# Performance work log

Measured on AMD Instinct MI355X. Metric: run time of the kernel, lower is better.

Reference implementation:

```python
import jax, jax.numpy as jnp
import numpy as np

E = 1024      # embed_size
H = 16        # num_heads
DH = E // H   # head_size = 64
B = 4
T = 2048


def _layernorm(x, g, b, eps=1e-5):
    mu = jnp.mean(x, axis=-1, keepdims=True)
    var = jnp.var(x, axis=-1, keepdims=True)
    return (x - mu) * jax.lax.rsqrt(var + eps) * g + b


def setup_inputs() -> dict:
    key = jax.random.key(0)
    ks = jax.random.split(key, 12)
    s = 0.02
    return {
        "x": jax.random.normal(ks[0], (B, T, E), dtype=jnp.float32),
        "ln1_g": jnp.ones((E,), jnp.float32),
        "ln1_b": jnp.zeros((E,), jnp.float32),
        "Wq": jax.random.normal(ks[1], (H, E, DH), jnp.float32) * s,
        "Wk": jax.random.normal(ks[2], (H, E, DH), jnp.float32) * s,
        "Wv": jax.random.normal(ks[3], (H, E, DH), jnp.float32) * s,
        "Wp": jax.random.normal(ks[4], (E, E), jnp.float32) * s,
        "bp": jnp.zeros((E,), jnp.float32),
        "ln2_g": jnp.ones((E,), jnp.float32),
        "ln2_b": jnp.zeros((E,), jnp.float32),
        "W1": jax.random.normal(ks[5], (E, 4 * E), jnp.float32) * s,
        "b1": jnp.zeros((4 * E,), jnp.float32),
        "W2": jax.random.normal(ks[6], (4 * E, E), jnp.float32) * s,
        "b2": jnp.zeros((E,), jnp.float32),
    }


def reference(x, ln1_g, ln1_b, Wq, Wk, Wv, Wp, bp, ln2_g, ln2_b, W1, b1, W2, b2):
    # --- self-attention branch (pre-LN) ---
    h = _layernorm(x, ln1_g, ln1_b)
    q = jnp.einsum("bte,hed->bhtd", h, Wq)
    k = jnp.einsum("bte,hed->bhtd", h, Wk)
    v = jnp.einsum("bte,hed->bhtd", h, Wv)
    # NOTE: original scales by embed_size**-0.5 (C of the input), not head_size
    scale = jnp.float32(E) ** -0.5
    w = jnp.einsum("bhtd,bhsd->bhts", q, k) * scale  # [B,H,T,T]
    causal = jnp.tril(jnp.ones((T, T), dtype=bool))
    w = jnp.where(causal, w, -jnp.inf)
    w = jax.nn.softmax(w, axis=-1)
    att = jnp.einsum("bhts,bhsd->bhtd", w, v)        # [B,H,T,DH]
    att = jnp.transpose(att, (0, 2, 1, 3)).reshape(B, T, E)  # concat heads
    x = x + att @ Wp + bp
    # --- FFN branch (pre-LN) ---
    h2 = _layernorm(x, ln2_g, ln2_b)
    ff = jax.nn.relu(h2 @ W1 + b1) @ W2 + b2
    return x + ff
```

## Files before the change

kernel.cpp:

```cpp
#include <hip/hip_runtime.h>
#include <stdint.h>

#define DEV __device__ __forceinline__

typedef unsigned short u16;
typedef short s16x8 __attribute__((ext_vector_type(8)));
typedef u16 u16x4 __attribute__((ext_vector_type(4)));
typedef float f32x4 __attribute__((ext_vector_type(4)));

constexpr int Bc = 4, Tc = 2048, Ec = 1024, Hc = 16, DHc = 64, FFc = 4096;

DEV u16 f2bf(float f) {
    union { float f; uint32_t u; } v; v.f = f;
    uint32_t r = v.u + 0x7fffu + ((v.u >> 16) & 1u);
    return (u16)(r >> 16);
}
DEV float bf2f(u16 u) {
    union { uint32_t u; float f; } v; v.u = ((uint32_t)u) << 16;
    return v.f;
}

DEV void gload16(const void* g, void* l) {
    __builtin_amdgcn_global_load_lds((const __attribute__((address_space(1))) void*)g,
                                     (__attribute__((address_space(3))) void*)l, 16, 0, 0);
}

template <typename TIN>
__global__ __launch_bounds__(256) void transpose_conv(const TIN* __restrict__ in,
                                                      u16* __restrict__ out, int R, int C) {
    __shared__ float tile[32][33];
    int bz = blockIdx.z;
    in  += (size_t)bz * R * C;
    out += (size_t)bz * R * C;
    int c0 = blockIdx.x * 32, r0 = blockIdx.y * 32;
    int tx = threadIdx.x, ty = threadIdx.y;
#pragma unroll
    for (int i = 0; i < 4; i++) {
        int r = ty + 8 * i;
        float v;
        if constexpr (sizeof(TIN) == 4) v = ((const float*)in)[(size_t)(r0 + r) * C + c0 + tx];
        else                            v = bf2f(((const u16*)in)[(size_t)(r0 + r) * C + c0 + tx]);
        tile[r][tx] = v;
    }
    __syncthreads();
#pragma unroll
    for (int i = 0; i < 4; i++) {
        int c = ty + 8 * i;
        out[(size_t)(c0 + c) * R + r0 + tx] = f2bf(tile[tx][c]);
    }
}

__global__ __launch_bounds__(256) void ln_kernel(const float* __restrict__ x, const float* __restrict__ g,
                                                 const float* __restrict__ b, u16* __restrict__ out) {
    int row = blockIdx.x;
    const float4* xr = (const float4*)(x + (size_t)row * Ec);
    int t = threadIdx.x;
    float4 v = xr[t];
    float s = v.x + v.y + v.z + v.w;
    float ss = v.x * v.x + v.y * v.y + v.z * v.z + v.w * v.w;
#pragma unroll
    for (int off = 32; off > 0; off >>= 1) { s += __shfl_xor(s, off); ss += __shfl_xor(ss, off); }
    __shared__ float red[8];
    int wid = t >> 6;
    if ((t & 63) == 0) { red[wid] = s; red[4 + wid] = ss; }
    __syncthreads();
    s = red[0] + red[1] + red[2] + red[3];
    ss = red[4] + red[5] + red[6] + red[7];
    float mu = s * (1.f / Ec);
    float rs = rsqrtf(ss * (1.f / Ec) - mu * mu + 1e-5f);
    float4 gv = ((const float4*)g)[t], bv = ((const float4*)b)[t];
    u16x4 o;
    o[0] = f2bf((v.x - mu) * rs * gv.x + bv.x);
    o[1] = f2bf((v.y - mu) * rs * gv.y + bv.y);
    o[2] = f2bf((v.z - mu) * rs * gv.z + bv.z);
    o[3] = f2bf((v.w - mu) * rs * gv.w + bv.w);
    *(u16x4*)(out + (size_t)row * Ec + t * 4) = o;
}

template <int MODE>
__global__ __launch_bounds__(256) void gemm_kernel(const u16* __restrict__ A, const u16* __restrict__ Bt,
                                                   int K, int N,
                                                   u16* __restrict__ o0, u16* __restrict__ o1, u16* __restrict__ o2,
                                                   float* __restrict__ of, const float* __restrict__ bias,
                                                   const float* __restrict__ res) {
    __shared__ u16 As[128 * 32];
    __shared__ u16 Bs[128 * 32];
    int tm = blockIdx.y * 128, tn = blockIdx.x * 128;
    int tid = threadIdx.x;
    int w = tid >> 6, l = tid & 63;
    int wm = w >> 1, wn = w & 1;
    int q16 = l & 15, g = l >> 4;

    f32x4 acc[4][4];
#pragma unroll
    for (int i = 0; i < 4; i++)
#pragma unroll
        for (int j = 0; j < 4; j++) acc[i][j] = {0.f, 0.f, 0.f, 0.f};

    const u16* Aw0 = A + (size_t)(tm + w * 32 + (l >> 2)) * K + (l & 3) * 8;
    const u16* Aw1 = Aw0 + (size_t)16 * K;
    const u16* Bw0 = Bt + (size_t)(tn + w * 32 + (l >> 2)) * K + (l & 3) * 8;
    const u16* Bw1 = Bw0 + (size_t)16 * K;
    u16* Asw = As + (w * 32) * 32;
    u16* Bsw = Bs + (w * 32) * 32;

    for (int k0 = 0; k0 < K; k0 += 32) {
        gload16(Aw0 + k0, Asw);
        gload16(Aw1 + k0, Asw + 16 * 32);
        gload16(Bw0 + k0, Bsw);
        gload16(Bw1 + k0, Bsw + 16 * 32);
        asm volatile("s_waitcnt vmcnt(0)" ::: "memory");
        __syncthreads();
        s16x8 af[4], bf[4];
#pragma unroll
        for (int i = 0; i < 4; i++) {
            af[i] = *(const s16x8*)(As + (wm * 64 + i * 16 + q16) * 32 + g * 8);
            bf[i] = *(const s16x8*)(Bs + (wn * 64 + i * 16 + q16) * 32 + g * 8);
        }
#pragma unroll
        for (int i = 0; i < 4; i++)
#pragma unroll
            for (int j = 0; j < 4; j++)
                acc[i][j] = __builtin_amdgcn_mfma_f32_16x16x32_bf16(af[i], bf[j], acc[i][j], 0, 0, 0);
        __syncthreads();
    }

#pragma unroll
    for (int i = 0; i < 4; i++) {
        int m0 = tm + wm * 64 + i * 16 + g * 4;
#pragma unroll
        for (int j = 0; j < 4; j++) {
            int n = tn + wn * 64 + j * 16 + q16;
            if constexpr (MODE == 0) {
                int tensor = n >> 10, hh = (n >> 6) & 15, d = n & 63;
                u16* dst = tensor == 0 ? o0 : (tensor == 1 ? o1 : o2);
#pragma unroll
                for (int r = 0; r < 4; r++) {
                    int m = m0 + r;
                    int bb = m >> 11, tt = m & 2047;
                    dst[(((size_t)(bb * Hc + hh) * Tc + tt) << 6) + d] = f2bf(acc[i][j][r]);
                }
            } else if constexpr (MODE == 1) {
                float bv = bias[n];
#pragma unroll
                for (int r = 0; r < 4; r++) {
                    int m = m0 + r;
                    o0[(size_t)m * N + n] = f2bf(fmaxf(acc[i][j][r] + bv, 0.f));
                }
            } else {
                float bv = bias[n];
#pragma unroll
                for (int r = 0; r < 4; r++) {
                    int m = m0 + r;
                    of[(size_t)m * N + n] = acc[i][j][r] + bv + res[(size_t)m * N + n];
                }
            }
        }
    }
}

__global__ __launch_bounds__(256) void attn_kernel(const u16* __restrict__ q, const u16* __restrict__ k,
                                                   const u16* __restrict__ vt, u16* __restrict__ att) {
    __shared__ u16 pt[4][32][72];
    int bh = blockIdx.y;
    int bb = bh >> 4, hh = bh & 15;
    int q0 = blockIdx.x * 128;
    int tid = threadIdx.x;
    int w = tid >> 6, l = tid & 63;
    int q16 = l & 15, g = l >> 4;

    const u16* Q  = q  + (size_t)bh * Tc * DHc;
    const u16* Kp = k  + (size_t)bh * Tc * DHc;
    const u16* Vt = vt + (size_t)bh * DHc * Tc;

    int qw = q0 + w * 32;

    s16x8 qf[2][2];
#pragma unroll
    for (int mf = 0; mf < 2; mf++)
#pragma unroll
        for (int c = 0; c < 2; c++)
            qf[mf][c] = *(const s16x8*)(Q + (size_t)(qw + mf * 16 + q16) * DHc + c * 32 + g * 8);

    f32x4 Of[4][2];
#pragma unroll
    for (int i = 0; i < 4; i++)
#pragma unroll
        for (int j = 0; j < 2; j++) Of[i][j] = {0.f, 0.f, 0.f, 0.f};
    float mrun[2] = {-1e30f, -1e30f};
    float lrun[2] = {0.f, 0.f};
    const float scale = 0.03125f;
    int qidx[2] = {qw + q16, qw + 16 + q16};

    int smax = qw + 32;
    for (int s0 = 0; s0 < smax; s0 += 64) {
        s16x8 kf[4][2];
#pragma unroll
        for (int sf = 0; sf < 4; sf++)
#pragma unroll
            for (int c = 0; c < 2; c++)
                kf[sf][c] = *(const s16x8*)(Kp + (size_t)(s0 + sf * 16 + q16) * DHc + c * 32 + g * 8);

        f32x4 sacc[4][2];
#pragma unroll
        for (int sf = 0; sf < 4; sf++)
#pragma unroll
            for (int j = 0; j < 2; j++) sacc[sf][j] = {0.f, 0.f, 0.f, 0.f};
#pragma unroll
        for (int sf = 0; sf < 4; sf++)
#pragma unroll
            for (int j = 0; j < 2; j++)
#pragma unroll
                for (int c = 0; c < 2; c++)
                    sacc[sf][j] = __builtin_amdgcn_mfma_f32_16x16x32_bf16(kf[sf][c], qf[j][c], sacc[sf][j], 0, 0, 0);

#pragma unroll
        for (int qfi = 0; qfi < 2; qfi++) {
            float pv[4][4];
            float tmax = -1e30f;
#pragma unroll
            for (int sf = 0; sf < 4; sf++)
#pragma unroll
                for (int r = 0; r < 4; r++) {
                    int s = s0 + sf * 16 + g * 4 + r;
                    float val = sacc[sf][qfi][r] * scale;
                    if (s > qidx[qfi]) val = -1e30f;
                    pv[sf][r] = val;
                    tmax = fmaxf(tmax, val);
                }
            tmax = fmaxf(tmax, __shfl_xor(tmax, 16));
            tmax = fmaxf(tmax, __shfl_xor(tmax, 32));
            float mnew = fmaxf(mrun[qfi], tmax);
            float alpha = __expf(mrun[qfi] - mnew);
            mrun[qfi] = mnew;
            float psum = 0.f;
#pragma unroll
            for (int sf = 0; sf < 4; sf++) {
                float p0 = __expf(pv[sf][0] - mnew);
                float p1 = __expf(pv[sf][1] - mnew);
                float p2 = __expf(pv[sf][2] - mnew);
                float p3 = __expf(pv[sf][3] - mnew);
                psum += p0 + p1 + p2 + p3;
                u16x4 pb;
                pb[0] = f2bf(p0); pb[1] = f2bf(p1); pb[2] = f2bf(p2); pb[3] = f2bf(p3);
                *(u16x4*)&pt[w][qfi * 16 + q16][sf * 16 + g * 4] = pb;
            }
            psum += __shfl_xor(psum, 16);
            psum += __shfl_xor(psum, 32);
            lrun[qfi] = lrun[qfi] * alpha + psum;
#pragma unroll
            for (int df = 0; df < 4; df++) {
                Of[df][qfi][0] *= alpha; Of[df][qfi][1] *= alpha;
                Of[df][qfi][2] *= alpha; Of[df][qfi][3] *= alpha;
            }
        }

#pragma unroll
        for (int c = 0; c < 2; c++) {
            s16x8 vf[4];
#pragma unroll
            for (int df = 0; df < 4; df++)
                vf[df] = *(const s16x8*)(Vt + (size_t)(df * 16 + q16) * Tc + s0 + c * 32 + g * 8);
#pragma unroll
            for (int qfi = 0; qfi < 2; qfi++) {
                s16x8 pb = *(const s16x8*)&pt[w][qfi * 16 + q16][c * 32 + g * 8];
#pragma unroll
                for (int df = 0; df < 4; df++)
                    Of[df][qfi] = __builtin_amdgcn_mfma_f32_16x16x32_bf16(vf[df], pb, Of[df][qfi], 0, 0, 0);
            }
        }
    }

#pragma unroll
    for (int qfi = 0; qfi < 2; qfi++) {
        float inv = 1.f / lrun[qfi];
        int tq = qw + qfi * 16 + q16;
#pragma unroll
        for (int df = 0; df < 4; df++) {
            u16x4 o;
            o[0] = f2bf(Of[df][qfi][0] * inv);
            o[1] = f2bf(Of[df][qfi][1] * inv);
            o[2] = f2bf(Of[df][qfi][2] * inv);
            o[3] = f2bf(Of[df][qfi][3] * inv);
            *(u16x4*)(att + ((size_t)(bb * Tc + tq)) * Ec + hh * 64 + df * 16 + g * 4) = o;
        }
    }
}

extern "C" void kernel_launch(void* const* d_in, const int* in_sizes, int n_in,
                              void* d_out, int out_size, void* d_ws, size_t ws_size,
                              hipStream_t stream) {
    (void)in_sizes; (void)n_in; (void)out_size; (void)ws_size;
    const float* x    = (const float*)d_in[0];
    const float* ln1g = (const float*)d_in[1];
    const float* ln1b = (const float*)d_in[2];
    const float* Wq   = (const float*)d_in[3];
    const float* Wk   = (const float*)d_in[4];
    const float* Wv   = (const float*)d_in[5];
    const float* Wp   = (const float*)d_in[6];
    const float* bp   = (const float*)d_in[7];
    const float* ln2g = (const float*)d_in[8];
    const float* ln2b = (const float*)d_in[9];
    const float* W1   = (const float*)d_in[10];
    const float* b1   = (const float*)d_in[11];
    const float* W2   = (const float*)d_in[12];
    const float* b2   = (const float*)d_in[13];
    float* out = (float*)d_out;
    char* ws = (char*)d_ws;

    u16*  wqkvt = (u16*)(ws + 0);
    u16*  wpt   = (u16*)(ws + 6291456);
    u16*  w1t   = (u16*)(ws + 8388608);
    u16*  w2t   = (u16*)(ws + 16777216);
    u16*  h     = (u16*)(ws + 25165824);
    u16*  att   = h;
    u16*  qb    = (u16*)(ws + 41943040);
    u16*  h2    = qb;
    u16*  kb    = (u16*)(ws + 58720256);
    u16*  vb    = (u16*)(ws + 75497472);
    u16*  vtb   = (u16*)(ws + 92274688);
    float* x2   = (float*)(ws + 109051904);
    u16*  ff1   = (u16*)(ws + 142606336);

    dim3 tb(32, 8);
    transpose_conv<float><<<dim3(2, 32, 16), tb, 0, stream>>>(Wq, wqkvt,            1024, 64);
    transpose_conv<float><<<dim3(2, 32, 16), tb, 0, stream>>>(Wk, wqkvt + 1048576,  1024, 64);
    transpose_conv<float><<<dim3(2, 32, 16), tb, 0, stream>>>(Wv, wqkvt + 2097152,  1024, 64);
    transpose_conv<float><<<dim3(32, 32, 1), tb, 0, stream>>>(Wp, wpt, 1024, 1024);
    transpose_conv<float><<<dim3(128, 32, 1), tb, 0, stream>>>(W1, w1t, 1024, 4096);
    transpose_conv<float><<<dim3(32, 128, 1), tb, 0, stream>>>(W2, w2t, 4096, 1024);

    ln_kernel<<<8192, 256, 0, stream>>>(x, ln1g, ln1b, h);

    gemm_kernel<0><<<dim3(24, 64), 256, 0, stream>>>(h, wqkvt, 1024, 3072, qb, kb, vb, nullptr, nullptr, nullptr);

    transpose_conv<u16><<<dim3(2, 64, 64), tb, 0, stream>>>(vb, vtb, 2048, 64);

    attn_kernel<<<dim3(16, 64), 256, 0, stream>>>(qb, kb, vtb, att);

    gemm_kernel<2><<<dim3(8, 64), 256, 0, stream>>>(att, wpt, 1024, 1024, nullptr, nullptr, nullptr, x2, bp, x);

    ln_kernel<<<8192, 256, 0, stream>>>(x2, ln2g, ln2b, h2);

    gemm_kernel<1><<<dim3(32, 64), 256, 0, stream>>>(h2, w1t, 1024, 4096, ff1, nullptr, nullptr, nullptr, b1, nullptr);

    gemm_kernel<2><<<dim3(8, 64), 256, 0, stream>>>(ff1, w2t, 4096, 1024, nullptr, nullptr, nullptr, out, b2, x2);
}
```

Measured before the change: 735.5 us.

## Stage K/V tiles through double-buffered LDS and write V transposed from QKV GEMM

```diff
diff --git a/kernel.cpp b/kernel.cpp
--- a/kernel.cpp
+++ b/kernel.cpp
@@ -133,12 +133,21 @@
             int n = tn + wn * 64 + j * 16 + q16;
             if constexpr (MODE == 0) {
                 int tensor = n >> 10, hh = (n >> 6) & 15, d = n & 63;
-                u16* dst = tensor == 0 ? o0 : (tensor == 1 ? o1 : o2);
-#pragma unroll
-                for (int r = 0; r < 4; r++) {
-                    int m = m0 + r;
-                    int bb = m >> 11, tt = m & 2047;
-                    dst[(((size_t)(bb * Hc + hh) * Tc + tt) << 6) + d] = f2bf(acc[i][j][r]);
+                if (tensor < 2) {
+                    u16* dst = tensor == 0 ? o0 : o1;
+#pragma unroll
+                    for (int r = 0; r < 4; r++) {
+                        int m = m0 + r;
+                        int bb = m >> 11, tt = m & 2047;
+                        dst[(((size_t)(bb * Hc + hh) * Tc + tt) << 6) + d] = f2bf(acc[i][j][r]);
+                    }
+                } else {
+#pragma unroll
+                    for (int r = 0; r < 4; r++) {
+                        int m = m0 + r;
+                        int bb = m >> 11, tt = m & 2047;
+                        o2[((size_t)(bb * Hc + hh) * DHc + d) * Tc + tt] = f2bf(acc[i][j][r]);
+                    }
                 }
             } else if constexpr (MODE == 1) {
                 float bv = bias[n];
@@ -161,10 +170,12 @@
 
 __global__ __launch_bounds__(256) void attn_kernel(const u16* __restrict__ q, const u16* __restrict__ k,
                                                    const u16* __restrict__ vt, u16* __restrict__ att) {
+    __shared__ u16 Ks[2][64 * 64];
+    __shared__ u16 Vs[2][64 * 64];
     __shared__ u16 pt[4][32][72];
     int bh = blockIdx.y;
     int bb = bh >> 4, hh = bh & 15;
-    int q0 = blockIdx.x * 128;
+    int q0 = (15 - blockIdx.x) * 128;
     int tid = threadIdx.x;
     int w = tid >> 6, l = tid & 63;
     int q16 = l & 15, g = l >> 4;
@@ -192,83 +203,108 @@
     const float scale = 0.03125f;
     int qidx[2] = {qw + q16, qw + 16 + q16};
 
-    int smax = qw + 32;
-    for (int s0 = 0; s0 < smax; s0 += 64) {
-        s16x8 kf[4][2];
-#pragma unroll
-        for (int sf = 0; sf < 4; sf++)
-#pragma unroll
-            for (int c = 0; c < 2; c++)
-                kf[sf][c] = *(const s16x8*)(Kp + (size_t)(s0 + sf * 16 + q16) * DHc + c * 32 + g * 8);
-
-        f32x4 sacc[4][2];
-#pragma unroll
-        for (int sf = 0; sf < 4; sf++)
-#pragma unroll
-            for (int j = 0; j < 2; j++) sacc[sf][j] = {0.f, 0.f, 0.f, 0.f};
-#pragma unroll
-        for (int sf = 0; sf < 4; sf++)
-#pragma unroll
-            for (int j = 0; j < 2; j++)
+    int ri = tid >> 3, sl = tid & 7;
+
+    auto stage = [&](int t, int bufi) {
+        int s0 = t * 64;
+        gload16(Kp + (size_t)(s0 + ri) * DHc + ((sl ^ (ri & 7)) << 3),        &Ks[bufi][w * 512]);
+        gload16(Kp + (size_t)(s0 + ri + 32) * DHc + ((sl ^ (ri & 7)) << 3),   &Ks[bufi][2048 + w * 512]);
+        gload16(Vt + (size_t)ri * Tc + s0 + ((sl ^ (ri & 7)) << 3),           &Vs[bufi][w * 512]);
+        gload16(Vt + (size_t)(ri + 32) * Tc + s0 + ((sl ^ (ri & 7)) << 3),    &Vs[bufi][2048 + w * 512]);
+    };
+
+    int nt = q0 / 64 + 2;
+    stage(0, 0);
+    for (int t = 0; t < nt; ++t) {
+        int cur = t & 1;
+        if (t + 1 < nt) {
+            stage(t + 1, cur ^ 1);
+            asm volatile("s_waitcnt vmcnt(4)" ::: "memory");
+        } else {
+            asm volatile("s_waitcnt vmcnt(0)" ::: "memory");
+        }
+        __syncthreads();
+        int s0 = t * 64;
+        if (s0 < qw + 32) {
+            const u16* Ksb = &Ks[cur][0];
+            const u16* Vsb = &Vs[cur][0];
+            s16x8 kf[4][2];
+#pragma unroll
+            for (int sf = 0; sf < 4; sf++)
 #pragma unroll
                 for (int c = 0; c < 2; c++)
-                    sacc[sf][j] = __builtin_amdgcn_mfma_f32_16x16x32_bf16(kf[sf][c], qf[j][c], sacc[sf][j], 0, 0, 0);
-
-#pragma unroll
-        for (int qfi = 0; qfi < 2; qfi++) {
-            float pv[4][4];
-            float tmax = -1e30f;
+                    kf[sf][c] = *(const s16x8*)(Ksb + (sf * 16 + q16) * 64 + (((c * 4 + g) ^ (q16 & 7)) << 3));
+
+            f32x4 sacc[4][2];
 #pragma unroll
             for (int sf = 0; sf < 4; sf++)
 #pragma unroll
-                for (int r = 0; r < 4; r++) {
-                    int s = s0 + sf * 16 + g * 4 + r;
-                    float val = sacc[sf][qfi][r] * scale;
-                    if (s > qidx[qfi]) val = -1e30f;
-                    pv[sf][r] = val;
-                    tmax = fmaxf(tmax, val);
-                }
-            tmax = fmaxf(tmax, __shfl_xor(tmax, 16));
-            tmax = fmaxf(tmax, __shfl_xor(tmax, 32));
-            float mnew = fmaxf(mrun[qfi], tmax);
-            float alpha = __expf(mrun[qfi] - mnew);
-            mrun[qfi] = mnew;
-            float psum = 0.f;
-#pragma unroll
-            for (int sf = 0; sf < 4; sf++) {
-                float p0 = __expf(pv[sf][0] - mnew);
-                float p1 = __expf(pv[sf][1] - mnew);
-                float p2 = __expf(pv[sf][2] - mnew);
-                float p3 = __expf(pv[sf][3] - mnew);
-                psum += p0 + p1 + p2 + p3;
-                u16x4 pb;
-                pb[0] = f2bf(p0); pb[1] = f2bf(p1); pb[2] = f2bf(p2); pb[3] = f2bf(p3);
-                *(u16x4*)&pt[w][qfi * 16 + q16][sf * 16 + g * 4] = pb;
+                for (int j = 0; j < 2; j++) sacc[sf][j] = {0.f, 0.f, 0.f, 0.f};
+#pragma unroll
+            for (int sf = 0; sf < 4; sf++)
+#pragma unroll
+                for (int j = 0; j < 2; j++)
+#pragma unroll
+                    for (int c = 0; c < 2; c++)
+                        sacc[sf][j] = __builtin_amdgcn_mfma_f32_16x16x32_bf16(kf[sf][c], qf[j][c], sacc[sf][j], 0, 0, 0);
+
+#pragma unroll
+            for (int qfi = 0; qfi < 2; qfi++) {
+                float pv[4][4];
+                float tmax = -1e30f;
+#pragma unroll
+                for (int sf = 0; sf < 4; sf++)
+#pragma unroll
+                    for (int r = 0; r < 4; r++) {
+                        int s = s0 + sf * 16 + g * 4 + r;
+                        float val = sacc[sf][qfi][r] * scale;
+                        if (s > qidx[qfi]) val = -1e30f;
+                        pv[sf][r] = val;
+                        tmax = fmaxf(tmax, val);
+                    }
+                tmax = fmaxf(tmax, __shfl_xor(tmax, 16));
+                tmax = fmaxf(tmax, __shfl_xor(tmax, 32));
+                float mnew = fmaxf(mrun[qfi], tmax);
+                float alpha = __expf(mrun[qfi] - mnew);
+                mrun[qfi] = mnew;
+                float psum = 0.f;
+#pragma unroll
+                for (int sf = 0; sf < 4; sf++) {
+                    float p0 = __expf(pv[sf][0] - mnew);
+                    float p1 = __expf(pv[sf][1] - mnew);
+                    float p2 = __expf(pv[sf][2] - mnew);
+                    float p3 = __expf(pv[sf][3] - mnew);
+                    psum += p0 + p1 + p2 + p3;
+                    u16x4 pb;
+                    pb[0] = f2bf(p0); pb[1] = f2bf(p1); pb[2] = f2bf(p2); pb[3] = f2bf(p3);
+                    *(u16x4*)&pt[w][qfi * 16 + q16][sf * 16 + g * 4] = pb;
+                }
+                psum += __shfl_xor(psum, 16);
+                psum += __shfl_xor(psum, 32);
+                lrun[qfi] = lrun[qfi] * alpha + psum;
+#pragma unroll
+                for (int df = 0; df < 4; df++) {
+                    Of[df][qfi][0] *= alpha; Of[df][qfi][1] *= alpha;
+                    Of[df][qfi][2] *= alpha; Of[df][qfi][3] *= alpha;
+                }
             }
-            psum += __shfl_xor(psum, 16);
-            psum += __shfl_xor(psum, 32);
-            lrun[qfi] = lrun[qfi] * alpha + psum;
-#pragma unroll
-            for (int df = 0; df < 4; df++) {
-                Of[df][qfi][0] *= alpha; Of[df][qfi][1] *= alpha;
-                Of[df][qfi][2] *= alpha; Of[df][qfi][3] *= alpha;
+
+#pragma unroll
+            for (int c = 0; c < 2; c++) {
+                s16x8 vf[4];
+#pragma unroll
+                for (int df = 0; df < 4; df++)
+                    vf[df] = *(const s16x8*)(Vsb + (df * 16 + q16) * 64 + (((c * 4 + g) ^ (q16 & 7)) << 3));
+#pragma unroll
+                for (int qfi = 0; qfi < 2; qfi++) {
+                    s16x8 pb = *(const s16x8*)&pt[w][qfi * 16 + q16][c * 32 + g * 8];
+#pragma unroll
+                    for (int df = 0; df < 4; df++)
+                        Of[df][qfi] = __builtin_amdgcn_mfma_f32_16x16x32_bf16(vf[df], pb, Of[df][qfi], 0, 0, 0);
+                }
             }
         }
-
-#pragma unroll
-        for (int c = 0; c < 2; c++) {
-            s16x8 vf[4];
-#pragma unroll
-            for (int df = 0; df < 4; df++)
-                vf[df] = *(const s16x8*)(Vt + (size_t)(df * 16 + q16) * Tc + s0 + c * 32 + g * 8);
-#pragma unroll
-            for (int qfi = 0; qfi < 2; qfi++) {
-                s16x8 pb = *(const s16x8*)&pt[w][qfi * 16 + q16][c * 32 + g * 8];
-#pragma unroll
-                for (int df = 0; df < 4; df++)
-                    Of[df][qfi] = __builtin_amdgcn_mfma_f32_16x16x32_bf16(vf[df], pb, Of[df][qfi], 0, 0, 0);
-            }
-        }
+        __syncthreads();
     }
 
 #pragma unroll
@@ -317,7 +353,6 @@
     u16*  qb    = (u16*)(ws + 41943040);
     u16*  h2    = qb;
     u16*  kb    = (u16*)(ws + 58720256);
-    u16*  vb    = (u16*)(ws + 75497472);
     u16*  vtb   = (u16*)(ws + 92274688);
     float* x2   = (float*)(ws + 109051904);
     u16*  ff1   = (u16*)(ws + 142606336);
@@ -332,9 +367,7 @@
 
     ln_kernel<<<8192, 256, 0, stream>>>(x, ln1g, ln1b, h);
 
-    gemm_kernel<0><<<dim3(24, 64), 256, 0, stream>>>(h, wqkvt, 1024, 3072, qb, kb, vb, nullptr, nullptr, nullptr);
-
-    transpose_conv<u16><<<dim3(2, 64, 64), tb, 0, stream>>>(vb, vtb, 2048, 64);
+    gemm_kernel<0><<<dim3(24, 64), 256, 0, stream>>>(h, wqkvt, 1024, 3072, qb, kb, vtb, nullptr, nullptr, nullptr);
 
     attn_kernel<<<dim3(16, 64), 256, 0, stream>>>(qb, kb, vtb, att);
 
```

After: 646.5 us. -12.1%, faster.
